# Kernel tuning notes

Hardware: AMD Instinct MI355X
Metric: run time of the kernel (lower is better)

Reference implementation:

```python
import math
import jax, jax.numpy as jnp
import numpy as np

# Constants (module-level in original repo; plausible biological values)
LATENCY_EPSILON = 1e-6
HAIR_CELL_COMPRESSION_EXPONENT = 0.3
HAIR_CELL_ADAPTATION_SUPPRESSION = 0.5
AUDITORY_NERVE_ADAPTATION_DECAY = 0.9
AUDITORY_NERVE_ADAPTATION_RATE = 0.1

SAMPLE_RATE = 16000
N_FFT = 512
N_FILTERS = 128
OUTPUT_SIZE = 262144
N_TIMESTEPS = 128
SPARSITY = 0.05
F_MIN, F_MAX = 80.0, 7600.0


def build_filterbank() -> np.ndarray:
    """Mel triangular filterbank, faithful to _create_filterbank (integer bin edges)."""
    hz_to_mel = lambda hz: 2595.0 * math.log10(1.0 + hz / 700.0)
    mel_to_hz = lambda mel: 700.0 * (10.0 ** (mel / 2595.0) - 1.0)
    mel_pts = np.linspace(hz_to_mel(F_MIN), hz_to_mel(F_MAX), N_FILTERS + 2)
    hz_pts = np.array([mel_to_hz(m) for m in mel_pts])
    bins = (hz_pts * N_FFT / SAMPLE_RATE).astype(np.int64)  # .long() truncation
    fb = np.zeros((N_FILTERS, N_FFT // 2 + 1), dtype=np.float32)
    for i in range(N_FILTERS):
        l, c, r = bins[i], bins[i + 1], bins[i + 2]
        for j in range(l, c):
            if c > l:
                fb[i, j] = (j - l) / (c - l)
        for j in range(c, r):
            if r > c:
                fb[i, j] = (r - j) / (r - c)
    return fb


def setup_inputs() -> dict:
    key = jax.random.key(0)
    k_audio, k_w = jax.random.split(key)
    audio = jax.random.normal(k_audio, (SAMPLE_RATE,), dtype=jnp.float32)
    filterbank = jnp.asarray(build_filterbank())  # [n_filters, n_fft//2+1]
    W = jax.random.normal(k_w, (OUTPUT_SIZE, N_FILTERS), dtype=jnp.float32) * 0.02
    b = jnp.zeros((OUTPUT_SIZE,), dtype=jnp.float32)
    adaptation_state = jnp.zeros((N_FILTERS,), dtype=jnp.float32)
    return {"audio": audio, "filterbank": filterbank, "W": W, "b": b,
            "adaptation_state": adaptation_state}


def reference(audio, filterbank, W, b, adaptation_state):
    # Basilar membrane: rfft with n=N_FFT (truncates audio to first N_FFT samples)
    spec = jnp.fft.rfft(audio, n=N_FFT)            # [n_fft//2+1] complex
    magnitude = jnp.abs(spec).astype(jnp.float32)   # [257]
    cochlear = filterbank @ magnitude               # [n_filters]
    # Hair cell compression
    hair = jnp.power(cochlear + LATENCY_EPSILON, HAIR_CELL_COMPRESSION_EXPONENT)
    adapted = jax.nn.relu(hair - adaptation_state * HAIR_CELL_ADAPTATION_SUPPRESSION)
    # Output projection (torch Linear: x @ W.T + b)
    activity = W @ adapted + b                      # [output_size]
    # Latency coding: high activity -> early spike (vectorized scatter)
    a_min, a_max = activity.min(), activity.max()
    norm = (activity - a_min) / (a_max - a_min + 1e-6)
    latencies = ((1.0 - norm) * (N_TIMESTEPS - 1)).astype(jnp.int32)  # [output_size]
    fire = norm > SPARSITY                           # [output_size]
    # spikes[t, n] = fire[n] and latencies[n] == t
    spikes = (latencies[None, :] == jnp.arange(N_TIMESTEPS, dtype=jnp.int32)[:, None]) \
             & fire[None, :]                         # [n_timesteps, output_size] bool
    return spikes
```

## Files before the change

### kernel.cpp

```cpp
#include <hip/hip_runtime.h>
#include <math.h>

#ifndef M_PI
#define M_PI 3.14159265358979323846
#endif

#define N_FFT       512
#define N_BINS      257
#define N_FILTERS   128
#define OUTPUT_SIZE 262144
#define N_TIMESTEPS 128

typedef int int4v __attribute__((ext_vector_type(4)));

__device__ __forceinline__ unsigned long long enc_d(double f) {
    unsigned long long u = (unsigned long long)__double_as_longlong(f);
    return (u & 0x8000000000000000ull) ? ~u : (u | 0x8000000000000000ull);
}
__device__ __forceinline__ double dec_d(unsigned long long e) {
    unsigned long long u = (e & 0x8000000000000000ull) ? (e ^ 0x8000000000000000ull) : ~e;
    return __longlong_as_double((long long)u);
}

__global__ __launch_bounds__(64) void k1a_dft(
    const float* __restrict__ audio, float* __restrict__ mag,
    unsigned long long* __restrict__ minmax)
{
    __shared__ double sre[64];
    __shared__ double sim[64];

    const int b    = blockIdx.x;
    const int lane = threadIdx.x;

    double re = 0.0, im = 0.0;
    #pragma unroll
    for (int j = 0; j < 8; ++j) {
        const int n = lane * 8 + j;
        const int m = (b * n) & (N_FFT - 1);
        double s, c;
        sincos((-2.0 * M_PI * (double)m) / (double)N_FFT, &s, &c);
        const double a = (double)audio[n];
        re += a * c;
        im += a * s;
    }
    sre[lane] = re;
    sim[lane] = im;
    __syncthreads();
    #pragma unroll
    for (int s = 32; s > 0; s >>= 1) {
        if (lane < s) {
            sre[lane] += sre[lane + s];
            sim[lane] += sim[lane + s];
        }
        __syncthreads();
    }
    if (lane == 0) {
        mag[b] = (float)sqrt(sre[0] * sre[0] + sim[0] * sim[0]);
        if (b == 0) {
            minmax[0] = 0xFFFFFFFFFFFFFFFFull;
            minmax[1] = 0ull;
        }
    }
}

__global__ __launch_bounds__(256) void k2_gemv(
    const float4* __restrict__ W4, const float* __restrict__ bias,
    const float* __restrict__ fb, const float* __restrict__ mag,
    const float* __restrict__ adapt, double* __restrict__ activity,
    unsigned long long* __restrict__ minmax)
{
    __shared__ float  magl[N_BINS];
    __shared__ double ad[N_FILTERS];
    __shared__ double red_min[256];
    __shared__ double red_max[256];

    const int tid = threadIdx.x;

    for (int j = tid; j < N_BINS; j += 256) magl[j] = mag[j];
    __syncthreads();

    if (tid < N_FILTERS) {
        double acc = 0.0;
        const float* row = fb + tid * N_BINS;
        #pragma unroll 4
        for (int j = 0; j < N_BINS; ++j)
            acc += (double)row[j] * (double)magl[j];
        const double x = acc + 1e-6;
        const double p = pow(x, 0.3);
        const double a = p - (double)adapt[tid] * 0.5;
        ad[tid] = a > 0.0 ? a : 0.0;
    }
    __syncthreads();

    const int row = blockIdx.x * 256 + tid;
    const float4* wrow = W4 + (size_t)row * (N_FILTERS / 4);

    double acc = 0.0;
    #pragma unroll 8
    for (int j = 0; j < N_FILTERS / 4; ++j) {
        float4 w = wrow[j];
        const int k = j * 4;
        acc += (double)w.x * ad[k];
        acc += (double)w.y * ad[k + 1];
        acc += (double)w.z * ad[k + 2];
        acc += (double)w.w * ad[k + 3];
    }
    double a = acc + (double)bias[row];
    activity[row] = a;

    red_min[tid] = a;
    red_max[tid] = a;
    __syncthreads();
    for (int s = 128; s > 0; s >>= 1) {
        if (tid < s) {
            red_min[tid] = fmin(red_min[tid], red_min[tid + s]);
            red_max[tid] = fmax(red_max[tid], red_max[tid + s]);
        }
        __syncthreads();
    }
    if (tid == 0) {
        atomicMin(&minmax[0], enc_d(red_min[0]));
        atomicMax(&minmax[1], enc_d(red_max[0]));
    }
}

__global__ __launch_bounds__(256) void k3_spikes(
    const double* __restrict__ activity,
    const unsigned long long* __restrict__ minmax,
    int4v* __restrict__ out4)
{
    const int tid = blockIdx.x * 256 + threadIdx.x;
    const double amin = dec_d(minmax[0]);
    const double amax = dec_d(minmax[1]);
    const double denom = (amax - amin) + 1e-6;

    const double nx = (activity[4 * tid + 0] - amin) / denom;
    const double ny = (activity[4 * tid + 1] - amin) / denom;
    const double nz = (activity[4 * tid + 2] - amin) / denom;
    const double nw = (activity[4 * tid + 3] - amin) / denom;

    const int lx = (int)((1.0 - nx) * 127.0);
    const int ly = (int)((1.0 - ny) * 127.0);
    const int lz = (int)((1.0 - nz) * 127.0);
    const int lw = (int)((1.0 - nw) * 127.0);

    const int vx = (nx > 0.05) ? 1 : 0;
    const int vy = (ny > 0.05) ? 1 : 0;
    const int vz = (nz > 0.05) ? 1 : 0;
    const int vw = (nw > 0.05) ? 1 : 0;

    const int t0 = blockIdx.y * (N_TIMESTEPS / 4);
    #pragma unroll 8
    for (int t = t0; t < t0 + N_TIMESTEPS / 4; ++t) {
        int4v v;
        v.x = (lx == t) ? vx : 0;
        v.y = (ly == t) ? vy : 0;
        v.z = (lz == t) ? vz : 0;
        v.w = (lw == t) ? vw : 0;
        out4[(size_t)t * (OUTPUT_SIZE / 4) + tid] = v;
    }
}

extern "C" void kernel_launch(void* const* d_in, const int* in_sizes, int n_in,
                              void* d_out, int out_size, void* d_ws, size_t ws_size,
                              hipStream_t stream) {
    (void)in_sizes; (void)n_in; (void)out_size; (void)ws_size;

    const float* audio = (const float*)d_in[0];
    const float* fb    = (const float*)d_in[1];
    const float* W     = (const float*)d_in[2];
    const float* bias  = (const float*)d_in[3];
    const float* adapt = (const float*)d_in[4];
    int* out = (int*)d_out;

    double* activity = (double*)d_ws;
    unsigned long long* minmax =
        (unsigned long long*)(activity + OUTPUT_SIZE);
    float* mag = (float*)(minmax + 2);

    k1a_dft<<<N_BINS, 64, 0, stream>>>(audio, mag, minmax);
    k2_gemv<<<OUTPUT_SIZE / 256, 256, 0, stream>>>(
        (const float4*)W, bias, fb, mag, adapt, activity, minmax);
    k3_spikes<<<dim3(OUTPUT_SIZE / 4 / 256, 4), 256, 0, stream>>>(
        activity, minmax, (int4v*)out);
}
```

Before: 304.7 us.

## Split GEMV rows across thread pairs with shuffle reduction and batched loads

```diff
diff --git a/kernel.cpp b/kernel.cpp
--- a/kernel.cpp
+++ b/kernel.cpp
@@ -80,11 +80,20 @@
     __syncthreads();
 
     if (tid < N_FILTERS) {
+        const float* row = fb + tid * N_BINS;
         double acc = 0.0;
-        const float* row = fb + tid * N_BINS;
-        #pragma unroll 4
-        for (int j = 0; j < N_BINS; ++j)
-            acc += (double)row[j] * (double)magl[j];
+        int j = 0;
+        #pragma unroll 1
+        for (int b = 0; b < 8; ++b) {
+            float r[32];
+            #pragma unroll
+            for (int u = 0; u < 32; ++u) r[u] = row[j + u];
+            #pragma unroll
+            for (int u = 0; u < 32; ++u)
+                acc += (double)r[u] * (double)magl[j + u];
+            j += 32;
+        }
+        acc += (double)row[256] * (double)magl[256];
         const double x = acc + 1e-6;
         const double p = pow(x, 0.3);
         const double a = p - (double)adapt[tid] * 0.5;
@@ -92,21 +101,30 @@
     }
     __syncthreads();
 
-    const int row = blockIdx.x * 256 + tid;
-    const float4* wrow = W4 + (size_t)row * (N_FILTERS / 4);
+    const int gtid = blockIdx.x * 256 + tid;
+    const int row  = gtid >> 1;
+    const int half = gtid & 1;
+    const float4* wrow = W4 + (size_t)row * (N_FILTERS / 4) + half * 16;
+
+    float4 w[16];
+    #pragma unroll
+    for (int j = 0; j < 16; ++j) w[j] = wrow[j];
 
     double acc = 0.0;
-    #pragma unroll 8
-    for (int j = 0; j < N_FILTERS / 4; ++j) {
-        float4 w = wrow[j];
-        const int k = j * 4;
-        acc += (double)w.x * ad[k];
-        acc += (double)w.y * ad[k + 1];
-        acc += (double)w.z * ad[k + 2];
-        acc += (double)w.w * ad[k + 3];
-    }
-    double a = acc + (double)bias[row];
-    activity[row] = a;
+    #pragma unroll
+    for (int j = 0; j < 16; ++j) {
+        const int k = half * 64 + j * 4;
+        acc += (double)w[j].x * ad[k];
+        acc += (double)w[j].y * ad[k + 1];
+        acc += (double)w[j].z * ad[k + 2];
+        acc += (double)w[j].w * ad[k + 3];
+    }
+
+    const double other = __shfl_xor(acc, 1, 64);
+    const double lo = half ? other : acc;
+    const double hi = half ? acc : other;
+    const double a = (lo + hi) + (double)bias[row];
+    if (!half) activity[row] = a;
 
     red_min[tid] = a;
     red_max[tid] = a;
@@ -179,7 +197,7 @@
     float* mag = (float*)(minmax + 2);
 
     k1a_dft<<<N_BINS, 64, 0, stream>>>(audio, mag, minmax);
-    k2_gemv<<<OUTPUT_SIZE / 256, 256, 0, stream>>>(
+    k2_gemv<<<OUTPUT_SIZE * 2 / 256, 256, 0, stream>>>(
         (const float4*)W, bias, fb, mag, adapt, activity, minmax);
     k3_spikes<<<dim3(OUTPUT_SIZE / 4 / 256, 4), 256, 0, stream>>>(
         activity, minmax, (int4v*)out);
```

After: 306.8 us. Within noise of the previous version (+0.7%).
